# Performance work log

Hardware: AMD Instinct MI355X
Metric: run time of the kernel (lower is better)

The kernel has to match this reference:

```python
import jax, jax.numpy as jnp
import numpy as np

EPSILON = 1e-8
NUM_STEPS = 1000
S_OFFSET = 0.0001
POWER = 2
CLIPMAX = 0.999
B = 1048576


def _schedule():
    t = jnp.arange(0, NUM_STEPS + 1, dtype=jnp.float32)
    f_t = jnp.cos(np.pi / 2 * (t / NUM_STEPS + S_OFFSET) / (1 + S_OFFSET)) ** POWER
    alpha_bars = f_t / f_t[0]
    betas = jnp.concatenate([jnp.zeros([1], jnp.float32), 1.0 - alpha_bars[1:] / alpha_bars[:-1]])
    betas = jnp.minimum(betas, CLIPMAX)
    sigmas = jnp.sqrt(betas[1:] * ((1.0 - alpha_bars[:-1]) / (1.0 - alpha_bars[1:])))
    sigmas = jnp.concatenate([jnp.zeros([1], jnp.float32), sigmas])
    return alpha_bars, betas, sigmas


def setup_inputs() -> dict:
    key = jax.random.key(0)
    k1, k2, k3, k4, k5 = jax.random.split(key, 5)
    lt = jax.random.normal(k1, (B, 6), dtype=jnp.float32)
    predicted_l0 = jax.random.normal(k2, (B, 6), dtype=jnp.float32)
    pred_lattice = jax.random.normal(k3, (B, 3, 3), dtype=jnp.float32)
    z_noise = jax.random.normal(k4, (B, 6), dtype=jnp.float32)  # torch.randn_like(lt), frozen
    t = jax.random.randint(k5, (B,), 0, NUM_STEPS, dtype=jnp.int64)
    alpha_bars, betas, sigmas = _schedule()
    return {
        "lt": lt,
        "predicted_l0": predicted_l0,
        "pred_lattice": pred_lattice,
        "alpha_bars": alpha_bars,
        "betas": betas,
        "sigmas": sigmas,
        "z_noise": z_noise,
        "t": t,
    }


def reference(lt, predicted_l0, pred_lattice, alpha_bars, betas, sigmas, z_noise, t):
    # VP_lattice.reverse
    alpha = 1.0 - betas[t]
    alpha = jnp.maximum(alpha, 1.0 - betas[-2])  # clamp_min
    alpha_bar = alpha_bars[t]
    sigma = sigmas[t][:, None]

    # polar_decomposition: only the symmetric factor L_tilda = V diag(S) V^T is used
    _, S, Vt = jnp.linalg.svd(pred_lattice, full_matrices=False)  # (B,3),(B,3,3)
    L = jnp.einsum("bji,bj,bjk->bik", Vt, S, Vt)  # Vt^T @ diag(S) @ Vt
    L = (L + jnp.swapaxes(L, 1, 2)) / 2  # symmetrize

    # symmetric_matrix_to_vector: upper triangular incl. diagonal
    vec = jnp.stack([L[:, 0, 0], L[:, 0, 1], L[:, 0, 2], L[:, 1, 1], L[:, 1, 2], L[:, 2, 2]], axis=1)

    predicted_noise = lt - (vec + predicted_l0) / 2
    z = jnp.where((t > 1)[:, None], z_noise, jnp.zeros_like(z_noise))
    coef = (1.0 / jnp.sqrt(alpha + EPSILON))[:, None]
    scale = ((1.0 - alpha) / jnp.sqrt(1.0 - alpha_bar + EPSILON))[:, None]
    return coef * (lt - scale * predicted_noise) + sigma * z
```

## Files before the change

### kernel.cpp

```cpp
#include <hip/hip_runtime.h>


#define NUM_STEPS 1000

typedef float  f4 __attribute__((ext_vector_type(4)));
typedef int    i4 __attribute__((ext_vector_type(4)));

__global__ __launch_bounds__(256) void vp_lattice_kernel(
    const float* __restrict__ lt,
    const float* __restrict__ pl0,
    const float* __restrict__ plat,
    const float* __restrict__ alpha_bars,
    const float* __restrict__ betas,
    const float* __restrict__ sigmas,
    const float* __restrict__ z_noise,
    const int*   __restrict__ t,
    float* __restrict__ out,
    int nquad)
{
    __shared__ float sCoef[NUM_STEPS + 1];
    __shared__ float sScale[NUM_STEPS + 1];
    __shared__ float sSig[NUM_STEPS + 1];
    {
        float beta_last = betas[NUM_STEPS - 1];
        for (int j = threadIdx.x; j <= NUM_STEPS; j += 256) {
            float alpha = 1.0f - fminf(betas[j], beta_last);
            sCoef[j]  = 1.0f / sqrtf(alpha + 1e-8f);
            sScale[j] = (1.0f - alpha) / sqrtf(1.0f - alpha_bars[j] + 1e-8f);
            sSig[j]   = (j > 1) ? sigmas[j] : 0.0f;
        }
    }

    int gid = blockIdx.x * blockDim.x + threadIdx.x;
    if (gid >= nquad) { __syncthreads(); return; }

    const f4* plat4 = reinterpret_cast<const f4*>(plat)    + (size_t)gid * 9;
    const f4* lt4   = reinterpret_cast<const f4*>(lt)      + (size_t)gid * 6;
    const f4* pl4   = reinterpret_cast<const f4*>(pl0)     + (size_t)gid * 6;
    const f4* zn4   = reinterpret_cast<const f4*>(z_noise) + (size_t)gid * 6;
    i4 tt = reinterpret_cast<const i4*>(t)[gid];

    f4 A4[9], L4[6], P4[6], Z4[6];
#pragma unroll
    for (int j = 0; j < 9; ++j) A4[j] = __builtin_nontemporal_load(&plat4[j]);
#pragma unroll
    for (int j = 0; j < 6; ++j) L4[j] = __builtin_nontemporal_load(&lt4[j]);
#pragma unroll
    for (int j = 0; j < 6; ++j) P4[j] = __builtin_nontemporal_load(&pl4[j]);
#pragma unroll
    for (int j = 0; j < 6; ++j) Z4[j] = __builtin_nontemporal_load(&zn4[j]);

    const float* Af = reinterpret_cast<const float*>(A4);
    const float* Lf = reinterpret_cast<const float*>(L4);
    const float* Pf = reinterpret_cast<const float*>(P4);
    const float* Zf = reinterpret_cast<const float*>(Z4);
    int tis[4] = {tt.x, tt.y, tt.z, tt.w};

    __syncthreads();

    float ov[24];
#pragma unroll
    for (int r = 0; r < 4; ++r) {
        const float* A = Af + r * 9;
        float a00 = A[0], a01 = A[1], a02 = A[2];
        float a10 = A[3], a11 = A[4], a12 = A[5];
        float a20 = A[6], a21 = A[7], a22 = A[8];

        float m00 = a00*a00 + a10*a10 + a20*a20;
        float m01 = a00*a01 + a10*a11 + a20*a21;
        float m02 = a00*a02 + a10*a12 + a20*a22;
        float m11 = a01*a01 + a11*a11 + a21*a21;
        float m12 = a01*a02 + a11*a12 + a21*a22;
        float m22 = a02*a02 + a12*a12 + a22*a22;

        float q  = (m00 + m11 + m22) * (1.0f/3.0f);
        float b00 = m00 - q, b11 = m11 - q, b22 = m22 - q;
        float p1 = m01*m01 + m02*m02 + m12*m12;
        float p2 = b00*b00 + b11*b11 + b22*b22 + 2.0f*p1;
        float p  = sqrtf(p2 * (1.0f/6.0f));
        float detB = b00*(b11*b22 - m12*m12)
                   - m01*(m01*b22 - m12*m02)
                   + m02*(m01*m12 - b11*m02);
        float pinv = 1.0f / fmaxf(p, 1e-20f);
        float rr = 0.5f * detB * pinv * pinv * pinv;
        rr = fminf(fmaxf(rr, -1.0f), 1.0f);
        float phi = acosf(rr) * (1.0f/3.0f);
        float mu1 = q + 2.0f*p*cosf(phi);
        float mu3 = q + 2.0f*p*cosf(phi + 2.0943951023931953f);
        float mu2 = 3.0f*q - mu1 - mu3;
        float l1 = sqrtf(fmaxf(mu1, 0.0f));
        float l2 = sqrtf(fmaxf(mu2, 0.0f));
        float l3 = sqrtf(fmaxf(mu3, 0.0f));

        float IU   = l1 + l2 + l3;
        float IIU  = l1*(l2 + l3) + l2*l3;
        float IIIU = l1*l2*l3;
        float denom = (l1 + l2) * (l1 + l3) * (l2 + l3);
        float dinv  = 1.0f / fmaxf(denom, 1e-25f);
        float sd = (IU*IU - IIU) * dinv;
        float td = IU * IIIU * dinv;
        float nd = -dinv;

        float mm00 = m00*m00 + m01*m01 + m02*m02;
        float mm01 = m00*m01 + m01*m11 + m02*m12;
        float mm02 = m00*m02 + m01*m12 + m02*m22;
        float mm11 = m01*m01 + m11*m11 + m12*m12;
        float mm12 = m01*m02 + m11*m12 + m12*m22;
        float mm22 = m02*m02 + m12*m12 + m22*m22;

        float vv[6];
        vv[0] = nd*mm00 + sd*m00 + td;
        vv[1] = nd*mm01 + sd*m01;
        vv[2] = nd*mm02 + sd*m02;
        vv[3] = nd*mm11 + sd*m11 + td;
        vv[4] = nd*mm12 + sd*m12;
        vv[5] = nd*mm22 + sd*m22 + td;

        int ti = tis[r];
        float coef  = sCoef[ti];
        float scale = sScale[ti];
        float sig   = sSig[ti];
#pragma unroll
        for (int c = 0; c < 6; ++c) {
            float lc = Lf[r*6 + c];
            float pn = lc - 0.5f * (vv[c] + Pf[r*6 + c]);
            ov[r*6 + c] = coef * (lc - scale * pn) + sig * Zf[r*6 + c];
        }
    }

    f4* out4 = reinterpret_cast<f4*>(out) + (size_t)gid * 6;
#pragma unroll
    for (int j = 0; j < 6; ++j) {
        f4 o = {ov[4*j], ov[4*j+1], ov[4*j+2], ov[4*j+3]};
        __builtin_nontemporal_store(o, &out4[j]);
    }
}

extern "C" void kernel_launch(void* const* d_in, const int* in_sizes, int n_in,
                              void* d_out, int out_size, void* d_ws, size_t ws_size,
                              hipStream_t stream) {
    const float* lt         = (const float*)d_in[0];
    const float* pl0        = (const float*)d_in[1];
    const float* plat       = (const float*)d_in[2];
    const float* alpha_bars = (const float*)d_in[3];
    const float* betas      = (const float*)d_in[4];
    const float* sigmas     = (const float*)d_in[5];
    const float* z_noise    = (const float*)d_in[6];
    const int*   t          = (const int*)d_in[7];
    float* out = (float*)d_out;

    int n = in_sizes[0] / 6;
    int nquad = n / 4;
    int block = 256;
    int grid = (nquad + block - 1) / block;
    vp_lattice_kernel<<<grid, block, 0, stream>>>(
        lt, pl0, plat, alpha_bars, betas, sigmas, z_noise, t, out, nquad);
}
```

Measured before the change: 186.3 us.

## Split fused kernel into sqrtm-vector kernel and epilogue kernel via workspace

Replaces the single fused kernel with two launches. The first computes the polar symmetric factor vector from pred_lattice into a workspace buffer. The second reads it back together with lt, pl0, z_noise and t to apply the reverse-step epilogue. Schedule coefficients are computed per element from global memory instead of a shared-memory table, and nontemporal loads and stores are dropped. This adds a full write and reread of the intermediate vector plus an extra launch, apparently in exchange for lower register pressure per kernel. A scalar fused fallback is kept for when the workspace is too small.

```diff
diff --git a/kernel.cpp b/kernel.cpp
--- a/kernel.cpp
+++ b/kernel.cpp
@@ -3,10 +3,152 @@
 
 #define NUM_STEPS 1000
 
-typedef float  f4 __attribute__((ext_vector_type(4)));
-typedef int    i4 __attribute__((ext_vector_type(4)));
-
-__global__ __launch_bounds__(256) void vp_lattice_kernel(
+typedef float f4 __attribute__((ext_vector_type(4)));
+
+__device__ __forceinline__ void sqrtm_vec(const float* A, float* vv)
+{
+    float a00 = A[0], a01 = A[1], a02 = A[2];
+    float a10 = A[3], a11 = A[4], a12 = A[5];
+    float a20 = A[6], a21 = A[7], a22 = A[8];
+
+    float m00 = a00*a00 + a10*a10 + a20*a20;
+    float m01 = a00*a01 + a10*a11 + a20*a21;
+    float m02 = a00*a02 + a10*a12 + a20*a22;
+    float m11 = a01*a01 + a11*a11 + a21*a21;
+    float m12 = a01*a02 + a11*a12 + a21*a22;
+    float m22 = a02*a02 + a12*a12 + a22*a22;
+
+    float q  = (m00 + m11 + m22) * (1.0f/3.0f);
+    float b00 = m00 - q, b11 = m11 - q, b22 = m22 - q;
+    float p1 = m01*m01 + m02*m02 + m12*m12;
+    float p2 = b00*b00 + b11*b11 + b22*b22 + 2.0f*p1;
+    float p  = sqrtf(p2 * (1.0f/6.0f));
+    float detB = b00*(b11*b22 - m12*m12)
+               - m01*(m01*b22 - m12*m02)
+               + m02*(m01*m12 - b11*m02);
+    float pinv = 1.0f / fmaxf(p, 1e-20f);
+    float rr = 0.5f * detB * pinv * pinv * pinv;
+    rr = fminf(fmaxf(rr, -1.0f), 1.0f);
+    float phi = acosf(rr) * (1.0f/3.0f);
+    float mu1 = q + 2.0f*p*cosf(phi);
+    float mu3 = q + 2.0f*p*cosf(phi + 2.0943951023931953f);
+    float mu2 = 3.0f*q - mu1 - mu3;
+    float l1 = sqrtf(fmaxf(mu1, 0.0f));
+    float l2 = sqrtf(fmaxf(mu2, 0.0f));
+    float l3 = sqrtf(fmaxf(mu3, 0.0f));
+
+    float IU   = l1 + l2 + l3;
+    float IIU  = l1*(l2 + l3) + l2*l3;
+    float IIIU = l1*l2*l3;
+    float denom = (l1 + l2) * (l1 + l3) * (l2 + l3);
+    float dinv  = 1.0f / fmaxf(denom, 1e-25f);
+    float sd = (IU*IU - IIU) * dinv;
+    float td = IU * IIIU * dinv;
+    float nd = -dinv;
+
+    float mm00 = m00*m00 + m01*m01 + m02*m02;
+    float mm01 = m00*m01 + m01*m11 + m02*m12;
+    float mm02 = m00*m02 + m01*m12 + m02*m22;
+    float mm11 = m01*m01 + m11*m11 + m12*m12;
+    float mm12 = m01*m02 + m11*m12 + m12*m22;
+    float mm22 = m02*m02 + m12*m12 + m22*m22;
+
+    vv[0] = nd*mm00 + sd*m00 + td;
+    vv[1] = nd*mm01 + sd*m01;
+    vv[2] = nd*mm02 + sd*m02;
+    vv[3] = nd*mm11 + sd*m11 + td;
+    vv[4] = nd*mm12 + sd*m12;
+    vv[5] = nd*mm22 + sd*m22 + td;
+}
+
+__global__ __launch_bounds__(256) void k1_vec(
+    const float* __restrict__ plat,
+    float* __restrict__ vec,
+    int nquad)
+{
+    int gid = blockIdx.x * blockDim.x + threadIdx.x;
+    if (gid >= nquad) return;
+
+    const f4* plat4 = reinterpret_cast<const f4*>(plat) + (size_t)gid * 9;
+    f4 A4[9];
+#pragma unroll
+    for (int j = 0; j < 9; ++j) A4[j] = plat4[j];
+    const float* Af = reinterpret_cast<const float*>(A4);
+
+    float ov[24];
+#pragma unroll
+    for (int r = 0; r < 4; ++r) sqrtm_vec(Af + r * 9, ov + r * 6);
+
+    f4* vec4 = reinterpret_cast<f4*>(vec) + (size_t)gid * 6;
+#pragma unroll
+    for (int j = 0; j < 6; ++j) {
+        f4 o = {ov[4*j], ov[4*j+1], ov[4*j+2], ov[4*j+3]};
+        vec4[j] = o;
+    }
+}
+
+__global__ __launch_bounds__(256) void k2_epilogue(
+    const float* __restrict__ lt,
+    const float* __restrict__ pl0,
+    const float* __restrict__ vec,
+    const float* __restrict__ z_noise,
+    const int*   __restrict__ t,
+    const float* __restrict__ alpha_bars,
+    const float* __restrict__ betas,
+    const float* __restrict__ sigmas,
+    float* __restrict__ out,
+    int npair)
+{
+    int gid = blockIdx.x * blockDim.x + threadIdx.x;
+    if (gid >= npair) return;
+
+    const f4* lt4 = reinterpret_cast<const f4*>(lt)      + (size_t)gid * 3;
+    const f4* pl4 = reinterpret_cast<const f4*>(pl0)     + (size_t)gid * 3;
+    const f4* vc4 = reinterpret_cast<const f4*>(vec)     + (size_t)gid * 3;
+    const f4* zn4 = reinterpret_cast<const f4*>(z_noise) + (size_t)gid * 3;
+    f4 L4[3], P4[3], V4[3], Z4[3];
+#pragma unroll
+    for (int j = 0; j < 3; ++j) L4[j] = lt4[j];
+#pragma unroll
+    for (int j = 0; j < 3; ++j) P4[j] = pl4[j];
+#pragma unroll
+    for (int j = 0; j < 3; ++j) V4[j] = vc4[j];
+#pragma unroll
+    for (int j = 0; j < 3; ++j) Z4[j] = zn4[j];
+    int2 tt = reinterpret_cast<const int2*>(t)[gid];
+
+    const float* Lf = reinterpret_cast<const float*>(L4);
+    const float* Pf = reinterpret_cast<const float*>(P4);
+    const float* Vf = reinterpret_cast<const float*>(V4);
+    const float* Zf = reinterpret_cast<const float*>(Z4);
+
+    float beta_last = betas[NUM_STEPS - 1];
+    float ov[12];
+#pragma unroll
+    for (int r = 0; r < 2; ++r) {
+        int ti = (r == 0) ? tt.x : tt.y;
+        float alpha = 1.0f - fminf(betas[ti], beta_last);
+        float ab    = alpha_bars[ti];
+        float sig   = (ti > 1) ? sigmas[ti] : 0.0f;
+        float coef  = 1.0f / sqrtf(alpha + 1e-8f);
+        float scale = (1.0f - alpha) / sqrtf(1.0f - ab + 1e-8f);
+#pragma unroll
+        for (int c = 0; c < 6; ++c) {
+            float lc = Lf[r*6 + c];
+            float pn = lc - 0.5f * (Vf[r*6 + c] + Pf[r*6 + c]);
+            ov[r*6 + c] = coef * (lc - scale * pn) + sig * Zf[r*6 + c];
+        }
+    }
+
+    f4* out4 = reinterpret_cast<f4*>(out) + (size_t)gid * 3;
+#pragma unroll
+    for (int j = 0; j < 3; ++j) {
+        f4 o = {ov[4*j], ov[4*j+1], ov[4*j+2], ov[4*j+3]};
+        out4[j] = o;
+    }
+}
+
+__global__ __launch_bounds__(256) void fused_kernel(
     const float* __restrict__ lt,
     const float* __restrict__ pl0,
     const float* __restrict__ plat,
@@ -16,123 +158,31 @@
     const float* __restrict__ z_noise,
     const int*   __restrict__ t,
     float* __restrict__ out,
-    int nquad)
-{
-    __shared__ float sCoef[NUM_STEPS + 1];
-    __shared__ float sScale[NUM_STEPS + 1];
-    __shared__ float sSig[NUM_STEPS + 1];
-    {
-        float beta_last = betas[NUM_STEPS - 1];
-        for (int j = threadIdx.x; j <= NUM_STEPS; j += 256) {
-            float alpha = 1.0f - fminf(betas[j], beta_last);
-            sCoef[j]  = 1.0f / sqrtf(alpha + 1e-8f);
-            sScale[j] = (1.0f - alpha) / sqrtf(1.0f - alpha_bars[j] + 1e-8f);
-            sSig[j]   = (j > 1) ? sigmas[j] : 0.0f;
-        }
-    }
-
-    int gid = blockIdx.x * blockDim.x + threadIdx.x;
-    if (gid >= nquad) { __syncthreads(); return; }
-
-    const f4* plat4 = reinterpret_cast<const f4*>(plat)    + (size_t)gid * 9;
-    const f4* lt4   = reinterpret_cast<const f4*>(lt)      + (size_t)gid * 6;
-    const f4* pl4   = reinterpret_cast<const f4*>(pl0)     + (size_t)gid * 6;
-    const f4* zn4   = reinterpret_cast<const f4*>(z_noise) + (size_t)gid * 6;
-    i4 tt = reinterpret_cast<const i4*>(t)[gid];
-
-    f4 A4[9], L4[6], P4[6], Z4[6];
-#pragma unroll
-    for (int j = 0; j < 9; ++j) A4[j] = __builtin_nontemporal_load(&plat4[j]);
-#pragma unroll
-    for (int j = 0; j < 6; ++j) L4[j] = __builtin_nontemporal_load(&lt4[j]);
-#pragma unroll
-    for (int j = 0; j < 6; ++j) P4[j] = __builtin_nontemporal_load(&pl4[j]);
-#pragma unroll
-    for (int j = 0; j < 6; ++j) Z4[j] = __builtin_nontemporal_load(&zn4[j]);
-
-    const float* Af = reinterpret_cast<const float*>(A4);
-    const float* Lf = reinterpret_cast<const float*>(L4);
-    const float* Pf = reinterpret_cast<const float*>(P4);
-    const float* Zf = reinterpret_cast<const float*>(Z4);
-    int tis[4] = {tt.x, tt.y, tt.z, tt.w};
-
-    __syncthreads();
-
-    float ov[24];
-#pragma unroll
-    for (int r = 0; r < 4; ++r) {
-        const float* A = Af + r * 9;
-        float a00 = A[0], a01 = A[1], a02 = A[2];
-        float a10 = A[3], a11 = A[4], a12 = A[5];
-        float a20 = A[6], a21 = A[7], a22 = A[8];
-
-        float m00 = a00*a00 + a10*a10 + a20*a20;
-        float m01 = a00*a01 + a10*a11 + a20*a21;
-        float m02 = a00*a02 + a10*a12 + a20*a22;
-        float m11 = a01*a01 + a11*a11 + a21*a21;
-        float m12 = a01*a02 + a11*a12 + a21*a22;
-        float m22 = a02*a02 + a12*a12 + a22*a22;
-
-        float q  = (m00 + m11 + m22) * (1.0f/3.0f);
-        float b00 = m00 - q, b11 = m11 - q, b22 = m22 - q;
-        float p1 = m01*m01 + m02*m02 + m12*m12;
-        float p2 = b00*b00 + b11*b11 + b22*b22 + 2.0f*p1;
-        float p  = sqrtf(p2 * (1.0f/6.0f));
-        float detB = b00*(b11*b22 - m12*m12)
-                   - m01*(m01*b22 - m12*m02)
-                   + m02*(m01*m12 - b11*m02);
-        float pinv = 1.0f / fmaxf(p, 1e-20f);
-        float rr = 0.5f * detB * pinv * pinv * pinv;
-        rr = fminf(fmaxf(rr, -1.0f), 1.0f);
-        float phi = acosf(rr) * (1.0f/3.0f);
-        float mu1 = q + 2.0f*p*cosf(phi);
-        float mu3 = q + 2.0f*p*cosf(phi + 2.0943951023931953f);
-        float mu2 = 3.0f*q - mu1 - mu3;
-        float l1 = sqrtf(fmaxf(mu1, 0.0f));
-        float l2 = sqrtf(fmaxf(mu2, 0.0f));
-        float l3 = sqrtf(fmaxf(mu3, 0.0f));
-
-        float IU   = l1 + l2 + l3;
-        float IIU  = l1*(l2 + l3) + l2*l3;
-        float IIIU = l1*l2*l3;
-        float denom = (l1 + l2) * (l1 + l3) * (l2 + l3);
-        float dinv  = 1.0f / fmaxf(denom, 1e-25f);
-        float sd = (IU*IU - IIU) * dinv;
-        float td = IU * IIIU * dinv;
-        float nd = -dinv;
-
-        float mm00 = m00*m00 + m01*m01 + m02*m02;
-        float mm01 = m00*m01 + m01*m11 + m02*m12;
-        float mm02 = m00*m02 + m01*m12 + m02*m22;
-        float mm11 = m01*m01 + m11*m11 + m12*m12;
-        float mm12 = m01*m02 + m11*m12 + m12*m22;
-        float mm22 = m02*m02 + m12*m12 + m22*m22;
-
-        float vv[6];
-        vv[0] = nd*mm00 + sd*m00 + td;
-        vv[1] = nd*mm01 + sd*m01;
-        vv[2] = nd*mm02 + sd*m02;
-        vv[3] = nd*mm11 + sd*m11 + td;
-        vv[4] = nd*mm12 + sd*m12;
-        vv[5] = nd*mm22 + sd*m22 + td;
-
-        int ti = tis[r];
-        float coef  = sCoef[ti];
-        float scale = sScale[ti];
-        float sig   = sSig[ti];
-#pragma unroll
-        for (int c = 0; c < 6; ++c) {
-            float lc = Lf[r*6 + c];
-            float pn = lc - 0.5f * (vv[c] + Pf[r*6 + c]);
-            ov[r*6 + c] = coef * (lc - scale * pn) + sig * Zf[r*6 + c];
-        }
-    }
-
-    f4* out4 = reinterpret_cast<f4*>(out) + (size_t)gid * 6;
-#pragma unroll
-    for (int j = 0; j < 6; ++j) {
-        f4 o = {ov[4*j], ov[4*j+1], ov[4*j+2], ov[4*j+3]};
-        __builtin_nontemporal_store(o, &out4[j]);
+    int n)
+{
+    int i = blockIdx.x * blockDim.x + threadIdx.x;
+    if (i >= n) return;
+
+    size_t b9 = (size_t)i * 9;
+    float A[9];
+#pragma unroll
+    for (int j = 0; j < 9; ++j) A[j] = plat[b9 + j];
+    float vv[6];
+    sqrtm_vec(A, vv);
+
+    int ti = t[i];
+    float beta_last = betas[NUM_STEPS - 1];
+    float alpha = 1.0f - fminf(betas[ti], beta_last);
+    float coef  = 1.0f / sqrtf(alpha + 1e-8f);
+    float scale = (1.0f - alpha) / sqrtf(1.0f - alpha_bars[ti] + 1e-8f);
+    float sig   = (ti > 1) ? sigmas[ti] : 0.0f;
+
+    size_t b6 = (size_t)i * 6;
+#pragma unroll
+    for (int c = 0; c < 6; ++c) {
+        float lc = lt[b6 + c];
+        float pn = lc - 0.5f * (vv[c] + pl0[b6 + c]);
+        out[b6 + c] = coef * (lc - scale * pn) + sig * z_noise[b6 + c];
     }
 }
 
@@ -150,9 +200,17 @@
     float* out = (float*)d_out;
 
     int n = in_sizes[0] / 6;
-    int nquad = n / 4;
-    int block = 256;
-    int grid = (nquad + block - 1) / block;
-    vp_lattice_kernel<<<grid, block, 0, stream>>>(
-        lt, pl0, plat, alpha_bars, betas, sigmas, z_noise, t, out, nquad);
-}
+    size_t vec_bytes = (size_t)n * 6 * sizeof(float);
+
+    if (ws_size >= vec_bytes) {
+        float* vec = (float*)d_ws;
+        int nquad = n / 4;
+        k1_vec<<<(nquad + 255) / 256, 256, 0, stream>>>(plat, vec, nquad);
+        int npair = n / 2;
+        k2_epilogue<<<(npair + 255) / 256, 256, 0, stream>>>(
+            lt, pl0, vec, z_noise, t, alpha_bars, betas, sigmas, out, npair);
+    } else {
+        fused_kernel<<<(n + 255) / 256, 256, 0, stream>>>(
+            lt, pl0, plat, alpha_bars, betas, sigmas, z_noise, t, out, n);
+    }
+}
```

Result: faster. 168.9 us (-9.3%).

## Process two rows per thread and compute schedule coefficients per element instead of LDS tables

Applied to the files above, without the earlier changes.

Each thread now handles two rows instead of four, which doubles the thread count and lowers register pressure. The per-block shared-memory precompute of coef, scale and sigma tables and its barrier are removed; each element gathers betas, alpha_bars and sigmas directly and computes the coefficients inline. Loads and stores switch from nontemporal to ordinary accesses, and plat is read as float2 because nine floats per row no longer fit float4 alignment for a pair. The cost is extra per-element sqrt/divide work and scattered global gathers from small tables, which should hit in cache.

```diff
diff --git a/kernel.cpp b/kernel.cpp
--- a/kernel.cpp
+++ b/kernel.cpp
@@ -3,8 +3,64 @@
 
 #define NUM_STEPS 1000
 
-typedef float  f4 __attribute__((ext_vector_type(4)));
-typedef int    i4 __attribute__((ext_vector_type(4)));
+typedef float f4 __attribute__((ext_vector_type(4)));
+typedef float f2 __attribute__((ext_vector_type(2)));
+
+__device__ __forceinline__ void sqrtm_vec(const float* A, float* vv)
+{
+    float a00 = A[0], a01 = A[1], a02 = A[2];
+    float a10 = A[3], a11 = A[4], a12 = A[5];
+    float a20 = A[6], a21 = A[7], a22 = A[8];
+
+    float m00 = a00*a00 + a10*a10 + a20*a20;
+    float m01 = a00*a01 + a10*a11 + a20*a21;
+    float m02 = a00*a02 + a10*a12 + a20*a22;
+    float m11 = a01*a01 + a11*a11 + a21*a21;
+    float m12 = a01*a02 + a11*a12 + a21*a22;
+    float m22 = a02*a02 + a12*a12 + a22*a22;
+
+    float q  = (m00 + m11 + m22) * (1.0f/3.0f);
+    float b00 = m00 - q, b11 = m11 - q, b22 = m22 - q;
+    float p1 = m01*m01 + m02*m02 + m12*m12;
+    float p2 = b00*b00 + b11*b11 + b22*b22 + 2.0f*p1;
+    float p  = sqrtf(p2 * (1.0f/6.0f));
+    float detB = b00*(b11*b22 - m12*m12)
+               - m01*(m01*b22 - m12*m02)
+               + m02*(m01*m12 - b11*m02);
+    float pinv = 1.0f / fmaxf(p, 1e-20f);
+    float rr = 0.5f * detB * pinv * pinv * pinv;
+    rr = fminf(fmaxf(rr, -1.0f), 1.0f);
+    float phi = acosf(rr) * (1.0f/3.0f);
+    float mu1 = q + 2.0f*p*cosf(phi);
+    float mu3 = q + 2.0f*p*cosf(phi + 2.0943951023931953f);
+    float mu2 = 3.0f*q - mu1 - mu3;
+    float l1 = sqrtf(fmaxf(mu1, 0.0f));
+    float l2 = sqrtf(fmaxf(mu2, 0.0f));
+    float l3 = sqrtf(fmaxf(mu3, 0.0f));
+
+    float IU   = l1 + l2 + l3;
+    float IIU  = l1*(l2 + l3) + l2*l3;
+    float IIIU = l1*l2*l3;
+    float denom = (l1 + l2) * (l1 + l3) * (l2 + l3);
+    float dinv  = 1.0f / fmaxf(denom, 1e-25f);
+    float sd = (IU*IU - IIU) * dinv;
+    float td = IU * IIIU * dinv;
+    float nd = -dinv;
+
+    float mm00 = m00*m00 + m01*m01 + m02*m02;
+    float mm01 = m00*m01 + m01*m11 + m02*m12;
+    float mm02 = m00*m02 + m01*m12 + m02*m22;
+    float mm11 = m01*m01 + m11*m11 + m12*m12;
+    float mm12 = m01*m02 + m11*m12 + m12*m22;
+    float mm22 = m02*m02 + m12*m12 + m22*m22;
+
+    vv[0] = nd*mm00 + sd*m00 + td;
+    vv[1] = nd*mm01 + sd*m01;
+    vv[2] = nd*mm02 + sd*m02;
+    vv[3] = nd*mm11 + sd*m11 + td;
+    vv[4] = nd*mm12 + sd*m12;
+    vv[5] = nd*mm22 + sd*m22 + td;
+}
 
 __global__ __launch_bounds__(256) void vp_lattice_kernel(
     const float* __restrict__ lt,
@@ -16,110 +72,47 @@
     const float* __restrict__ z_noise,
     const int*   __restrict__ t,
     float* __restrict__ out,
-    int nquad)
+    int npair)
 {
-    __shared__ float sCoef[NUM_STEPS + 1];
-    __shared__ float sScale[NUM_STEPS + 1];
-    __shared__ float sSig[NUM_STEPS + 1];
-    {
-        float beta_last = betas[NUM_STEPS - 1];
-        for (int j = threadIdx.x; j <= NUM_STEPS; j += 256) {
-            float alpha = 1.0f - fminf(betas[j], beta_last);
-            sCoef[j]  = 1.0f / sqrtf(alpha + 1e-8f);
-            sScale[j] = (1.0f - alpha) / sqrtf(1.0f - alpha_bars[j] + 1e-8f);
-            sSig[j]   = (j > 1) ? sigmas[j] : 0.0f;
-        }
-    }
+    int gid = blockIdx.x * blockDim.x + threadIdx.x;
+    if (gid >= npair) return;
 
-    int gid = blockIdx.x * blockDim.x + threadIdx.x;
-    if (gid >= nquad) { __syncthreads(); return; }
+    const f4* lt4 = reinterpret_cast<const f4*>(lt)      + (size_t)gid * 3;
+    const f4* pl4 = reinterpret_cast<const f4*>(pl0)     + (size_t)gid * 3;
+    const f4* zn4 = reinterpret_cast<const f4*>(z_noise) + (size_t)gid * 3;
+    const f2* pp  = reinterpret_cast<const f2*>(plat)    + (size_t)gid * 9;
 
-    const f4* plat4 = reinterpret_cast<const f4*>(plat)    + (size_t)gid * 9;
-    const f4* lt4   = reinterpret_cast<const f4*>(lt)      + (size_t)gid * 6;
-    const f4* pl4   = reinterpret_cast<const f4*>(pl0)     + (size_t)gid * 6;
-    const f4* zn4   = reinterpret_cast<const f4*>(z_noise) + (size_t)gid * 6;
-    i4 tt = reinterpret_cast<const i4*>(t)[gid];
+    f4 L4[3], P4[3], Z4[3];
+    f2 A2[9];
+#pragma unroll
+    for (int j = 0; j < 3; ++j) L4[j] = lt4[j];
+#pragma unroll
+    for (int j = 0; j < 3; ++j) P4[j] = pl4[j];
+#pragma unroll
+    for (int j = 0; j < 3; ++j) Z4[j] = zn4[j];
+#pragma unroll
+    for (int j = 0; j < 9; ++j) A2[j] = pp[j];
+    int2 tt = reinterpret_cast<const int2*>(t)[gid];
 
-    f4 A4[9], L4[6], P4[6], Z4[6];
-#pragma unroll
-    for (int j = 0; j < 9; ++j) A4[j] = __builtin_nontemporal_load(&plat4[j]);
-#pragma unroll
-    for (int j = 0; j < 6; ++j) L4[j] = __builtin_nontemporal_load(&lt4[j]);
-#pragma unroll
-    for (int j = 0; j < 6; ++j) P4[j] = __builtin_nontemporal_load(&pl4[j]);
-#pragma unroll
-    for (int j = 0; j < 6; ++j) Z4[j] = __builtin_nontemporal_load(&zn4[j]);
-
-    const float* Af = reinterpret_cast<const float*>(A4);
     const float* Lf = reinterpret_cast<const float*>(L4);
     const float* Pf = reinterpret_cast<const float*>(P4);
     const float* Zf = reinterpret_cast<const float*>(Z4);
-    int tis[4] = {tt.x, tt.y, tt.z, tt.w};
+    const float* Af = reinterpret_cast<const float*>(A2);
 
-    __syncthreads();
+    float beta_last = betas[NUM_STEPS - 1];
 
-    float ov[24];
+    float ov[12];
 #pragma unroll
-    for (int r = 0; r < 4; ++r) {
-        const float* A = Af + r * 9;
-        float a00 = A[0], a01 = A[1], a02 = A[2];
-        float a10 = A[3], a11 = A[4], a12 = A[5];
-        float a20 = A[6], a21 = A[7], a22 = A[8];
+    for (int r = 0; r < 2; ++r) {
+        float vv[6];
+        sqrtm_vec(Af + r * 9, vv);
 
-        float m00 = a00*a00 + a10*a10 + a20*a20;
-        float m01 = a00*a01 + a10*a11 + a20*a21;
-        float m02 = a00*a02 + a10*a12 + a20*a22;
-        float m11 = a01*a01 + a11*a11 + a21*a21;
-        float m12 = a01*a02 + a11*a12 + a21*a22;
-        float m22 = a02*a02 + a12*a12 + a22*a22;
-
-        float q  = (m00 + m11 + m22) * (1.0f/3.0f);
-        float b00 = m00 - q, b11 = m11 - q, b22 = m22 - q;
-        float p1 = m01*m01 + m02*m02 + m12*m12;
-        float p2 = b00*b00 + b11*b11 + b22*b22 + 2.0f*p1;
-        float p  = sqrtf(p2 * (1.0f/6.0f));
-        float detB = b00*(b11*b22 - m12*m12)
-                   - m01*(m01*b22 - m12*m02)
-                   + m02*(m01*m12 - b11*m02);
-        float pinv = 1.0f / fmaxf(p, 1e-20f);
-        float rr = 0.5f * detB * pinv * pinv * pinv;
-        rr = fminf(fmaxf(rr, -1.0f), 1.0f);
-        float phi = acosf(rr) * (1.0f/3.0f);
-        float mu1 = q + 2.0f*p*cosf(phi);
-        float mu3 = q + 2.0f*p*cosf(phi + 2.0943951023931953f);
-        float mu2 = 3.0f*q - mu1 - mu3;
-        float l1 = sqrtf(fmaxf(mu1, 0.0f));
-        float l2 = sqrtf(fmaxf(mu2, 0.0f));
-        float l3 = sqrtf(fmaxf(mu3, 0.0f));
-
-        float IU   = l1 + l2 + l3;
-        float IIU  = l1*(l2 + l3) + l2*l3;
-        float IIIU = l1*l2*l3;
-        float denom = (l1 + l2) * (l1 + l3) * (l2 + l3);
-        float dinv  = 1.0f / fmaxf(denom, 1e-25f);
-        float sd = (IU*IU - IIU) * dinv;
-        float td = IU * IIIU * dinv;
-        float nd = -dinv;
-
-        float mm00 = m00*m00 + m01*m01 + m02*m02;
-        float mm01 = m00*m01 + m01*m11 + m02*m12;
-        float mm02 = m00*m02 + m01*m12 + m02*m22;
-        float mm11 = m01*m01 + m11*m11 + m12*m12;
-        float mm12 = m01*m02 + m11*m12 + m12*m22;
-        float mm22 = m02*m02 + m12*m12 + m22*m22;
-
-        float vv[6];
-        vv[0] = nd*mm00 + sd*m00 + td;
-        vv[1] = nd*mm01 + sd*m01;
-        vv[2] = nd*mm02 + sd*m02;
-        vv[3] = nd*mm11 + sd*m11 + td;
-        vv[4] = nd*mm12 + sd*m12;
-        vv[5] = nd*mm22 + sd*m22 + td;
-
-        int ti = tis[r];
-        float coef  = sCoef[ti];
-        float scale = sScale[ti];
-        float sig   = sSig[ti];
+        int ti = (r == 0) ? tt.x : tt.y;
+        float alpha = 1.0f - fminf(betas[ti], beta_last);
+        float ab    = alpha_bars[ti];
+        float sig   = (ti > 1) ? sigmas[ti] : 0.0f;
+        float coef  = 1.0f / sqrtf(alpha + 1e-8f);
+        float scale = (1.0f - alpha) / sqrtf(1.0f - ab + 1e-8f);
 #pragma unroll
         for (int c = 0; c < 6; ++c) {
             float lc = Lf[r*6 + c];
@@ -128,11 +121,11 @@
         }
     }
 
-    f4* out4 = reinterpret_cast<f4*>(out) + (size_t)gid * 6;
+    f4* out4 = reinterpret_cast<f4*>(out) + (size_t)gid * 3;
 #pragma unroll
-    for (int j = 0; j < 6; ++j) {
+    for (int j = 0; j < 3; ++j) {
         f4 o = {ov[4*j], ov[4*j+1], ov[4*j+2], ov[4*j+3]};
-        __builtin_nontemporal_store(o, &out4[j]);
+        out4[j] = o;
     }
 }
 
@@ -150,9 +143,9 @@
     float* out = (float*)d_out;
 
     int n = in_sizes[0] / 6;
-    int nquad = n / 4;
+    int npair = n / 2;
     int block = 256;
-    int grid = (nquad + block - 1) / block;
+    int grid = (npair + block - 1) / block;
     vp_lattice_kernel<<<grid, block, 0, stream>>>(
-        lt, pl0, plat, alpha_bars, betas, sigmas, z_noise, t, out, nquad);
+        lt, pl0, plat, alpha_bars, betas, sigmas, z_noise, t, out, npair);
 }
```

After: 155.0 us. 16.8% less time.
